# Optimization experiments

Hardware: AMD Instinct MI355X
Metric: run time of the kernel (lower is better)

## Reference

```python
import jax, jax.numpy as jnp
import numpy as np

HIDDEN = 1024
HEADS = 16
HEAD_DIM = HIDDEN // HEADS


def setup_inputs() -> dict:
    key = jax.random.key(0)
    k_x, k_wa, k_ba, k_wp, k_bp = jax.random.split(key, 5)
    x = jax.random.normal(k_x, (2, 2048, HIDDEN), dtype=jnp.float32)
    s_a = 1.0 / np.sqrt(HIDDEN)
    # torch Linear default init ~ U(-1/sqrt(fan_in), 1/sqrt(fan_in)); stored as [in, out]
    W_attn = jax.random.uniform(k_wa, (HIDDEN, 3 * HIDDEN), jnp.float32, -s_a, s_a)
    b_attn = jax.random.uniform(k_ba, (3 * HIDDEN,), jnp.float32, -s_a, s_a)
    W_proj = jax.random.uniform(k_wp, (HIDDEN, HIDDEN), jnp.float32, -s_a, s_a)
    b_proj = jax.random.uniform(k_bp, (HIDDEN,), jnp.float32, -s_a, s_a)
    return {"x": x, "W_attn": W_attn, "b_attn": b_attn, "W_proj": W_proj, "b_proj": b_proj}


def reference(x, W_attn, b_attn, W_proj, b_proj):
    B, S, D = x.shape
    H, Hd = HEADS, HEAD_DIM
    qkv = x @ W_attn + b_attn                     # [B, S, 3D]
    q, k, v = jnp.split(qkv, 3, axis=-1)
    # [B, H, S, Hd]
    q = q.reshape(B, S, H, Hd).transpose(0, 2, 1, 3)
    k = k.reshape(B, S, H, Hd).transpose(0, 2, 1, 3)
    v = v.reshape(B, S, H, Hd).transpose(0, 2, 1, 3)
    scale = 1.0 / np.sqrt(Hd).astype(np.float32)
    scores = jnp.einsum('bhqd,bhkd->bhqk', q, k) * scale   # [B, H, S, S]
    causal = jnp.triu(jnp.ones((S, S), dtype=bool), k=1)   # True above diagonal
    scores = jnp.where(causal, -jnp.inf, scores)
    probs = jax.nn.softmax(scores, axis=-1)
    # dropout p=0.0 -> identity (eval-mode equivalent)
    ctx = jnp.einsum('bhqk,bhkd->bhqd', probs, v)           # [B, H, S, Hd]
    ctx = ctx.transpose(0, 2, 1, 3).reshape(B, S, D)
    return ctx @ W_proj + b_proj
```

## Files before the change

kernel.cpp:

```cpp
#include <hip/hip_runtime.h>
#include <hip/hip_bf16.h>
#include <stdint.h>

#define HID 1024
#define NH 16
#define HD 64
#define SEQ 2048
#define BATCH 2
#define M_TOT 4096
#define QSCALE 0.18033688011112042f

typedef __attribute__((ext_vector_type(8))) short short8;
typedef __attribute__((ext_vector_type(4))) float f32x4;
typedef __attribute__((ext_vector_type(16))) float f32x16;
typedef __hip_bfloat16 bf16;

__device__ __forceinline__ void load_lds16(const void* g, void* l) {
  __builtin_amdgcn_global_load_lds(
      (const __attribute__((address_space(1))) unsigned int*)g,
      (__attribute__((address_space(3))) unsigned int*)l, 16, 0, 0);
}

__device__ __forceinline__ unsigned short f2bf_bits(float f) {
  __hip_bfloat16 h = __float2bfloat16(f);
  return *reinterpret_cast<unsigned short*>(&h);
}
__device__ __forceinline__ unsigned pack2bf(float a, float b) {
  return (unsigned)f2bf_bits(a) | ((unsigned)f2bf_bits(b) << 16);
}
__device__ __forceinline__ unsigned cvt_pk_bf16(float a, float b) {
  unsigned r;
  asm("v_cvt_pk_bf16_f32 %0, %1, %2" : "=v"(r) : "v"(a), "v"(b));
  return r;
}

__global__ void cvt_f32_to_bf16(const float* __restrict__ in,
                                bf16* __restrict__ out, int n4) {
  int i = blockIdx.x * blockDim.x + threadIdx.x;
  if (i >= n4) return;
  float4 v = reinterpret_cast<const float4*>(in)[i];
  ushort4 o;
  o.x = f2bf_bits(v.x); o.y = f2bf_bits(v.y);
  o.z = f2bf_bits(v.z); o.w = f2bf_bits(v.w);
  reinterpret_cast<ushort4*>(out)[i] = o;
}

__global__ void transpose_cvt2(const float* __restrict__ Wa, bf16* __restrict__ WTa,
                               const float* __restrict__ Wp, bf16* __restrict__ WTp) {
  __shared__ float tile[32][33];
  int bx = blockIdx.x;
  const float* W; bf16* WT; int N;
  if (bx < 96) { W = Wa; WT = WTa; N = 3072; }
  else         { W = Wp; WT = WTp; N = 1024; bx -= 96; }
  const int K = 1024;
  int n0 = bx * 32, k0 = blockIdx.y * 32;
  int tx = threadIdx.x, ty = threadIdx.y;
#pragma unroll
  for (int i = 0; i < 32; i += 8)
    tile[ty + i][tx] = W[(size_t)(k0 + ty + i) * N + n0 + tx];
  __syncthreads();
#pragma unroll
  for (int i = 0; i < 32; i += 8)
    WT[(size_t)(n0 + ty + i) * K + k0 + tx] = __float2bfloat16(tile[tx][ty + i]);
}

template <int EPI>
__global__ __launch_bounds__(256, 2)
void gemm128(const bf16* __restrict__ A, const bf16* __restrict__ BT,
             const float* __restrict__ bias,
             bf16* __restrict__ Qo, bf16* __restrict__ Ko, bf16* __restrict__ Vo,
             float* __restrict__ Fo) {
  const int Kdim = 1024;
  __shared__ bf16 As[128 * 64];
  __shared__ bf16 Bs[128 * 64];
  const int tid = threadIdx.x;
  const int wid = tid >> 6, lane = tid & 63;
  const int m0 = blockIdx.x * 128;
  const int n0 = blockIdx.y * 128;
  const int wrow = (wid >> 1) * 64, wcol = (wid & 1) * 64;

  f32x4 acc[4][4];
#pragma unroll
  for (int rb = 0; rb < 4; ++rb)
#pragma unroll
    for (int cb = 0; cb < 4; ++cb)
      acc[rb][cb] = (f32x4){0.f, 0.f, 0.f, 0.f};

  const int lr = lane >> 3;
  const int cc = lane & 7;
  const int lc = cc * 8;
  const int fr = lane & 15, fk = (lane >> 4) * 8;

  for (int kt = 0; kt < Kdim / 64; ++kt) {
    __syncthreads();
#pragma unroll
    for (int t = 0; t < 4; ++t) {
      int i = wid * 4 + t;
      int row = i * 8 + lr;
      load_lds16(A + (size_t)(m0 + row) * Kdim + kt * 64 + lc, (char*)As + i * 1024);
      load_lds16(BT + (size_t)(n0 + row) * Kdim + kt * 64 + lc, (char*)Bs + i * 1024);
    }
    __syncthreads();

    short8 af[4][2], bf_[4][2];
#pragma unroll
    for (int rb = 0; rb < 4; ++rb)
#pragma unroll
      for (int kk = 0; kk < 2; ++kk) {
        af[rb][kk] = *(const short8*)&As[(wrow + rb * 16 + fr) * 64 + kk * 32 + fk];
        bf_[rb][kk] = *(const short8*)&Bs[(wcol + rb * 16 + fr) * 64 + kk * 32 + fk];
      }
#pragma unroll
    for (int rb = 0; rb < 4; ++rb)
#pragma unroll
      for (int cb = 0; cb < 4; ++cb)
#pragma unroll
        for (int kk = 0; kk < 2; ++kk)
          acc[rb][cb] = __builtin_amdgcn_mfma_f32_16x16x32_bf16(
              af[rb][kk], bf_[cb][kk], acc[rb][cb], 0, 0, 0);
  }

  const int fg = (lane >> 4) * 4;
  float bv[4];
#pragma unroll
  for (int cb = 0; cb < 4; ++cb) bv[cb] = bias[n0 + wcol + cb * 16 + fr];

  if (EPI == 0) {
    __syncthreads();
    char* ep = (wid < 2 ? (char*)As : (char*)Bs) + (wid & 1) * 8192;
    const int ncol = n0 + wcol;
    const int part = ncol >> 10;
    const int h = (ncol & 1023) >> 6;
    const int b = m0 >> 11;
    const int s_base = (m0 + wrow) & 2047;
    const size_t hb = (size_t)(b * NH + h);

    if (part < 2) {
      const float qs = (part == 0) ? QSCALE : 1.f;
#pragma unroll
      for (int rb = 0; rb < 4; ++rb)
#pragma unroll
        for (int cb = 0; cb < 4; ++cb)
#pragma unroll
          for (int j = 0; j < 4; ++j) {
            int row = rb * 16 + fg + j;
            int colb = (cb * 16 + fr) * 2;
            *(unsigned short*)(ep + row * 128 + (colb ^ ((row & 7) << 4))) =
                f2bf_bits((acc[rb][cb][j] + bv[cb]) * qs);
          }
      bf16* dst = (part == 0 ? Qo : Ko) + hb * SEQ * HD;
#pragma unroll
      for (int p = 0; p < 8; ++p) {
        int row = p * 8 + lr;
        uint4 v = *(const uint4*)(ep + row * 128 + ((cc * 16) ^ ((row & 7) << 4)));
        *(uint4*)(dst + (size_t)(s_base + row) * HD + cc * 8) = v;
      }
    } else {
#pragma unroll
      for (int rb = 0; rb < 4; ++rb)
#pragma unroll
        for (int cb = 0; cb < 4; ++cb) {
          int cV = cb * 16 + fr;
          int r0 = (rb * 16 + fg) * 2;
          uint2 wv;
          wv.x = pack2bf(acc[rb][cb][0] + bv[cb], acc[rb][cb][1] + bv[cb]);
          wv.y = pack2bf(acc[rb][cb][2] + bv[cb], acc[rb][cb][3] + bv[cb]);
          *(uint2*)(ep + cV * 128 + (r0 ^ ((cV & 7) << 4))) = wv;
        }
      bf16* dstV = Vo + hb * HD * SEQ;
#pragma unroll
      for (int p = 0; p < 8; ++p) {
        int hd = p * 8 + lr;
        uint4 v = *(const uint4*)(ep + hd * 128 + ((cc * 16) ^ ((hd & 7) << 4)));
        *(uint4*)(dstV + (size_t)hd * SEQ + s_base + cc * 8) = v;
      }
    }
  } else {
#pragma unroll
    for (int rb = 0; rb < 4; ++rb) {
      int r0 = m0 + wrow + rb * 16 + fg;
#pragma unroll
      for (int cb = 0; cb < 4; ++cb) {
        int n = n0 + wcol + cb * 16 + fr;
#pragma unroll
        for (int j = 0; j < 4; ++j)
          Fo[(size_t)(r0 + j) * HID + n] = acc[rb][cb][j] + bv[cb];
      }
    }
  }
}

__global__ __launch_bounds__(256, 2)
void attn_kernel(const bf16* __restrict__ Q, const bf16* __restrict__ K,
                 const bf16* __restrict__ VT, bf16* __restrict__ ctx) {
  __shared__ char smem[65536];
  const int tid = threadIdx.x, wid = tid >> 6, lane = tid & 63;
  const int idx = blockIdx.x;
  const int qt = (idx < 256) ? (15 - (idx >> 5)) : ((idx - 256) >> 5);
  const int bh = idx & 31;
  const int b = bh >> 4, h = bh & 15;
  const size_t base = (size_t)bh * SEQ * HD;
  const int q0 = qt * 128 + wid * 32;

  const int fr = lane & 31, hi = lane >> 5;
  const int lr = lane >> 3;
  const int cc = lane & 7;
  const int qg = q0 + fr;
  const int gc = (cc ^ lr) * 8;

  short8 qf[4];
  const bf16* qp = Q + base + (size_t)qg * HD;
#pragma unroll
  for (int kc = 0; kc < 4; ++kc)
    qf[kc] = *(const short8*)(qp + kc * 16 + hi * 8);

  f32x16 oa[2], ob[2];
#pragma unroll
  for (int da = 0; da < 2; ++da)
#pragma unroll
    for (int r = 0; r < 16; ++r) { oa[da][r] = 0.f; ob[da][r] = 0.f; }
  float lpart = 0.f;

  auto stage_pair = [&](int jp) {
    char* nb = smem + (jp & 1) * 32768;
    const int nv = jp * 128;
#pragma unroll
    for (int u = 0; u < 2; ++u)
#pragma unroll
      for (int t = 0; t < 2; ++t) {
        int i = wid * 2 + t;
        load_lds16(K + base + (size_t)(nv + u * 64 + i * 8 + lr) * HD + gc,
                   nb + u * 16384 + i * 1024);
        load_lds16(VT + base + (size_t)(i * 8 + lr) * SEQ + nv + u * 64 + gc,
                   nb + u * 16384 + 8192 + i * 1024);
      }
  };

  auto tile_compute = [&](const char* sb_t, int kv0, f32x16 (&oc)[2]) {
    f32x16 sa[2];
    __builtin_amdgcn_s_setprio(1);
#pragma unroll
    for (int kb = 0; kb < 2; ++kb) {
#pragma unroll
      for (int r = 0; r < 16; ++r) sa[kb][r] = 0.f;
      const int row = kb * 32 + fr;
      const int swz = (row & 7) << 4;
#pragma unroll
      for (int kc = 0; kc < 4; ++kc) {
        short8 kf = *(const short8*)(sb_t + row * 128 + ((kc * 32 + hi * 16) ^ swz));
        sa[kb] = __builtin_amdgcn_mfma_f32_32x32x16_bf16(kf, qf[kc], sa[kb], 0, 0, 0);
      }
    }
    __builtin_amdgcn_s_setprio(0);

    if (kv0 + 63 > q0) {
#pragma unroll
      for (int kb = 0; kb < 2; ++kb)
#pragma unroll
        for (int r = 0; r < 16; ++r) {
          int kvg = kv0 + kb * 32 + (r & 3) + 8 * (r >> 2) + 4 * hi;
          sa[kb][r] = (kvg > qg) ? -1e30f : sa[kb][r];
        }
    }

    float s0 = 0.f, s1 = 0.f, s2 = 0.f, s3 = 0.f;
#pragma unroll
    for (int kb = 0; kb < 2; ++kb)
#pragma unroll
      for (int r = 0; r < 16; ++r) {
        float e = __builtin_exp2f(sa[kb][r]);
        sa[kb][r] = e;
        if ((r & 3) == 0)      s0 += e;
        else if ((r & 3) == 1) s1 += e;
        else if ((r & 3) == 2) s2 += e;
        else                   s3 += e;
      }
    lpart += (s0 + s1) + (s2 + s3);

    unsigned pk[2][8];
#pragma unroll
    for (int kb = 0; kb < 2; ++kb)
#pragma unroll
      for (int i = 0; i < 8; ++i)
        pk[kb][i] = cvt_pk_bf16(sa[kb][2 * i], sa[kb][2 * i + 1]);

    short8 pfr[4];
#pragma unroll
    for (int ks = 0; ks < 4; ++ks) {
      const int kb = ks >> 1, g = (ks & 1) * 4;
      auto r0 = __builtin_amdgcn_permlane32_swap((int)pk[kb][g + 0],
                                                 (int)pk[kb][g + 2], false, false);
      auto r1 = __builtin_amdgcn_permlane32_swap((int)pk[kb][g + 1],
                                                 (int)pk[kb][g + 3], false, false);
      union { unsigned u[4]; short8 s; } pf;
      pf.u[0] = (unsigned)r0[0]; pf.u[1] = (unsigned)r1[0];
      pf.u[2] = (unsigned)r0[1]; pf.u[3] = (unsigned)r1[1];
      pfr[ks] = pf.s;
    }

    __builtin_amdgcn_s_setprio(1);
#pragma unroll
    for (int da = 0; da < 2; ++da) {
      const int row = da * 32 + fr;
      const int swz = (row & 7) << 4;
#pragma unroll
      for (int ks = 0; ks < 4; ++ks) {
        short8 vf = *(const short8*)(sb_t + 8192 + row * 128 +
                                     ((ks * 32 + hi * 16) ^ swz));
        oc[da] = __builtin_amdgcn_mfma_f32_32x32x16_bf16(vf, pfr[ks], oc[da], 0, 0, 0);
      }
    }
    __builtin_amdgcn_s_setprio(0);
  };

  const int npair = qt + 1;

  stage_pair(0);

  for (int j = 0; j < npair; ++j) {
    char* sb = smem + (j & 1) * 32768;

    __builtin_amdgcn_s_barrier();
    __builtin_amdgcn_sched_barrier(0);

    if (j + 1 < npair) {
      stage_pair(j + 1);
      asm volatile("s_waitcnt vmcnt(8)" ::: "memory");
    } else {
      asm volatile("s_waitcnt vmcnt(0)" ::: "memory");
    }
    __builtin_amdgcn_sched_barrier(0);

    __builtin_amdgcn_s_barrier();
    __builtin_amdgcn_sched_barrier(0);

    const int kv0 = j * 128;
    if (kv0 <= q0 + 31)      tile_compute(sb,         kv0,      oa);
    if (kv0 + 64 <= q0 + 31) tile_compute(sb + 16384, kv0 + 64, ob);
  }

  const float lrun = lpart + __shfl_xor(lpart, 32);
  const float inv = 1.f / lrun;
  char* ep = smem + wid * 4096;
#pragma unroll
  for (int da = 0; da < 2; ++da)
#pragma unroll
    for (int rg = 0; rg < 4; ++rg) {
      int d0 = da * 64 + rg * 16 + hi * 8;
      float v0 = (oa[da][rg * 4 + 0] + ob[da][rg * 4 + 0]) * inv;
      float v1 = (oa[da][rg * 4 + 1] + ob[da][rg * 4 + 1]) * inv;
      float v2 = (oa[da][rg * 4 + 2] + ob[da][rg * 4 + 2]) * inv;
      float v3 = (oa[da][rg * 4 + 3] + ob[da][rg * 4 + 3]) * inv;
      uint2 wv; wv.x = pack2bf(v0, v1); wv.y = pack2bf(v2, v3);
      *(uint2*)(ep + fr * 128 + (d0 ^ ((fr & 7) << 4))) = wv;
    }
#pragma unroll
  for (int p = 0; p < 4; ++p) {
    int qr = p * 8 + lr;
    uint4 v = *(const uint4*)(ep + qr * 128 + ((cc * 16) ^ ((qr & 7) << 4)));
    int s = q0 + qr;
    *(uint4*)(ctx + (size_t)(b * SEQ + s) * HID + h * 64 + cc * 8) = v;
  }
}

extern "C" void kernel_launch(void* const* d_in, const int* in_sizes, int n_in,
                              void* d_out, int out_size, void* d_ws, size_t ws_size,
                              hipStream_t stream) {
  const float* x      = (const float*)d_in[0];
  const float* W_attn = (const float*)d_in[1];
  const float* b_attn = (const float*)d_in[2];
  const float* W_proj = (const float*)d_in[3];
  const float* b_proj = (const float*)d_in[4];
  float* out = (float*)d_out;

  char* ws = (char*)d_ws;
  const size_t MB = 1u << 20;
  bf16* xb   = (bf16*)(ws + 0);
  bf16* WTa  = (bf16*)(ws + 8 * MB);
  bf16* WTp  = (bf16*)(ws + 14 * MB);
  bf16* Qw   = (bf16*)(ws + 16 * MB);
  bf16* Kw   = (bf16*)(ws + 24 * MB);
  bf16* VTw  = (bf16*)(ws + 32 * MB);
  bf16* ctxb = (bf16*)(ws + 40 * MB);

  cvt_f32_to_bf16<<<(M_TOT * HID / 4 + 255) / 256, 256, 0, stream>>>(x, xb, M_TOT * HID / 4);
  transpose_cvt2<<<dim3(128, 32), dim3(32, 8), 0, stream>>>(W_attn, WTa, W_proj, WTp);

  gemm128<0><<<dim3(M_TOT / 128, 3 * HID / 128), 256, 0, stream>>>(
      xb, WTa, b_attn, Qw, Kw, VTw, nullptr);

  attn_kernel<<<dim3(512), 256, 0, stream>>>(Qw, Kw, VTw, ctxb);

  gemm128<1><<<dim3(M_TOT / 128, HID / 128), 256, 0, stream>>>(
      ctxb, WTp, b_proj, nullptr, nullptr, nullptr, out);
}
```

Measured before the change: 109.3 us.

## Shrink attention tiles to 64 queries with 16x16x32 MFMA and LDS-staged P

Restructures the attention kernel so each block handles 64 query rows instead of 128, with each wave owning 16 rows and using 16x16x32 bf16 MFMAs instead of 32x32x16. The grid doubles to 1024 blocks, LDS drops to 40 KB and launch bounds allow 4 blocks per CU, aiming for better occupancy and finer causal load balance. The probability fragment is now passed through LDS rather than permlane swaps, and K/V staging goes one 64-key tile at a time. The cost is more K/V reloads per query, since each KV tile is now reused across fewer queries, plus extra LDS traffic for P.

```diff
diff --git a/kernel.cpp b/kernel.cpp
--- a/kernel.cpp
+++ b/kernel.cpp
@@ -12,7 +12,6 @@
 
 typedef __attribute__((ext_vector_type(8))) short short8;
 typedef __attribute__((ext_vector_type(4))) float f32x4;
-typedef __attribute__((ext_vector_type(16))) float f32x16;
 typedef __hip_bfloat16 bf16;
 
 __device__ __forceinline__ void load_lds16(const void* g, void* l) {
@@ -190,142 +189,131 @@
   }
 }
 
-__global__ __launch_bounds__(256, 2)
+__global__ __launch_bounds__(256, 4)
 void attn_kernel(const bf16* __restrict__ Q, const bf16* __restrict__ K,
                  const bf16* __restrict__ VT, bf16* __restrict__ ctx) {
-  __shared__ char smem[65536];
+  __shared__ char smem[40960];
   const int tid = threadIdx.x, wid = tid >> 6, lane = tid & 63;
   const int idx = blockIdx.x;
-  const int qt = (idx < 256) ? (15 - (idx >> 5)) : ((idx - 256) >> 5);
+  const int qt = (idx < 512) ? (31 - (idx >> 5)) : ((idx - 512) >> 5);
   const int bh = idx & 31;
   const int b = bh >> 4, h = bh & 15;
   const size_t base = (size_t)bh * SEQ * HD;
-  const int q0 = qt * 128 + wid * 32;
-
-  const int fr = lane & 31, hi = lane >> 5;
+  const int q0 = qt * 64 + wid * 16;
+
+  const int fr16 = lane & 15, hi4 = lane >> 4;
   const int lr = lane >> 3;
   const int cc = lane & 7;
-  const int qg = q0 + fr;
+  const int qg = q0 + fr16;
   const int gc = (cc ^ lr) * 8;
-
-  short8 qf[4];
+  const int pswz = (fr16 & 7) << 4;
+  char* pp = smem + 32768 + wid * 2048;
+
+  short8 qf[2];
   const bf16* qp = Q + base + (size_t)qg * HD;
 #pragma unroll
-  for (int kc = 0; kc < 4; ++kc)
-    qf[kc] = *(const short8*)(qp + kc * 16 + hi * 8);
-
-  f32x16 oa[2], ob[2];
-#pragma unroll
-  for (int da = 0; da < 2; ++da)
-#pragma unroll
-    for (int r = 0; r < 16; ++r) { oa[da][r] = 0.f; ob[da][r] = 0.f; }
+  for (int kc = 0; kc < 2; ++kc)
+    qf[kc] = *(const short8*)(qp + kc * 32 + hi4 * 8);
+
+  f32x4 oa[4], ob[4];
+#pragma unroll
+  for (int dg = 0; dg < 4; ++dg) {
+    oa[dg] = (f32x4){0.f, 0.f, 0.f, 0.f};
+    ob[dg] = (f32x4){0.f, 0.f, 0.f, 0.f};
+  }
   float lpart = 0.f;
 
-  auto stage_pair = [&](int jp) {
-    char* nb = smem + (jp & 1) * 32768;
-    const int nv = jp * 128;
-#pragma unroll
-    for (int u = 0; u < 2; ++u)
-#pragma unroll
-      for (int t = 0; t < 2; ++t) {
-        int i = wid * 2 + t;
-        load_lds16(K + base + (size_t)(nv + u * 64 + i * 8 + lr) * HD + gc,
-                   nb + u * 16384 + i * 1024);
-        load_lds16(VT + base + (size_t)(i * 8 + lr) * SEQ + nv + u * 64 + gc,
-                   nb + u * 16384 + 8192 + i * 1024);
-      }
+  auto stage_tile = [&](int tt) {
+    char* nb = smem + (tt & 1) * 16384;
+    const int nv = tt * 64;
+#pragma unroll
+    for (int t = 0; t < 4; ++t) {
+      int c = wid * 4 + t;
+      if (c < 8)
+        load_lds16(K + base + (size_t)(nv + c * 8 + lr) * HD + gc, nb + c * 1024);
+      else
+        load_lds16(VT + base + (size_t)((c - 8) * 8 + lr) * SEQ + nv + gc,
+                   nb + 8192 + (c - 8) * 1024);
+    }
   };
 
-  auto tile_compute = [&](const char* sb_t, int kv0, f32x16 (&oc)[2]) {
-    f32x16 sa[2];
+  auto tile_compute = [&](const char* sb, int kv0, f32x4 (&oc)[4]) {
+    f32x4 sa[4];
     __builtin_amdgcn_s_setprio(1);
 #pragma unroll
-    for (int kb = 0; kb < 2; ++kb) {
-#pragma unroll
-      for (int r = 0; r < 16; ++r) sa[kb][r] = 0.f;
-      const int row = kb * 32 + fr;
+    for (int kb = 0; kb < 4; ++kb) {
+      sa[kb] = (f32x4){0.f, 0.f, 0.f, 0.f};
+      const int row = kb * 16 + fr16;
       const int swz = (row & 7) << 4;
 #pragma unroll
-      for (int kc = 0; kc < 4; ++kc) {
-        short8 kf = *(const short8*)(sb_t + row * 128 + ((kc * 32 + hi * 16) ^ swz));
-        sa[kb] = __builtin_amdgcn_mfma_f32_32x32x16_bf16(kf, qf[kc], sa[kb], 0, 0, 0);
+      for (int kc = 0; kc < 2; ++kc) {
+        short8 kf = *(const short8*)(sb + row * 128 + ((kc * 64 + hi4 * 16) ^ swz));
+        sa[kb] = __builtin_amdgcn_mfma_f32_16x16x32_bf16(kf, qf[kc], sa[kb], 0, 0, 0);
       }
     }
     __builtin_amdgcn_s_setprio(0);
 
     if (kv0 + 63 > q0) {
 #pragma unroll
-      for (int kb = 0; kb < 2; ++kb)
-#pragma unroll
-        for (int r = 0; r < 16; ++r) {
-          int kvg = kv0 + kb * 32 + (r & 3) + 8 * (r >> 2) + 4 * hi;
-          sa[kb][r] = (kvg > qg) ? -1e30f : sa[kb][r];
+      for (int kb = 0; kb < 4; ++kb)
+#pragma unroll
+        for (int j = 0; j < 4; ++j) {
+          int kvg = kv0 + kb * 16 + hi4 * 4 + j;
+          sa[kb][j] = (kvg > qg) ? -1e30f : sa[kb][j];
         }
     }
 
     float s0 = 0.f, s1 = 0.f, s2 = 0.f, s3 = 0.f;
 #pragma unroll
-    for (int kb = 0; kb < 2; ++kb)
-#pragma unroll
-      for (int r = 0; r < 16; ++r) {
-        float e = __builtin_exp2f(sa[kb][r]);
-        sa[kb][r] = e;
-        if ((r & 3) == 0)      s0 += e;
-        else if ((r & 3) == 1) s1 += e;
-        else if ((r & 3) == 2) s2 += e;
-        else                   s3 += e;
-      }
+    for (int kb = 0; kb < 4; ++kb) {
+      float e0 = __builtin_exp2f(sa[kb][0]);
+      float e1 = __builtin_exp2f(sa[kb][1]);
+      float e2 = __builtin_exp2f(sa[kb][2]);
+      float e3 = __builtin_exp2f(sa[kb][3]);
+      sa[kb][0] = e0; sa[kb][1] = e1; sa[kb][2] = e2; sa[kb][3] = e3;
+      s0 += e0; s1 += e1; s2 += e2; s3 += e3;
+    }
     lpart += (s0 + s1) + (s2 + s3);
 
-    unsigned pk[2][8];
-#pragma unroll
-    for (int kb = 0; kb < 2; ++kb)
-#pragma unroll
-      for (int i = 0; i < 8; ++i)
-        pk[kb][i] = cvt_pk_bf16(sa[kb][2 * i], sa[kb][2 * i + 1]);
-
-    short8 pfr[4];
-#pragma unroll
-    for (int ks = 0; ks < 4; ++ks) {
-      const int kb = ks >> 1, g = (ks & 1) * 4;
-      auto r0 = __builtin_amdgcn_permlane32_swap((int)pk[kb][g + 0],
-                                                 (int)pk[kb][g + 2], false, false);
-      auto r1 = __builtin_amdgcn_permlane32_swap((int)pk[kb][g + 1],
-                                                 (int)pk[kb][g + 3], false, false);
-      union { unsigned u[4]; short8 s; } pf;
-      pf.u[0] = (unsigned)r0[0]; pf.u[1] = (unsigned)r1[0];
-      pf.u[2] = (unsigned)r0[1]; pf.u[3] = (unsigned)r1[1];
-      pfr[ks] = pf.s;
-    }
-
+#pragma unroll
+    for (int kb = 0; kb < 4; ++kb) {
+      uint2 u;
+      u.x = cvt_pk_bf16(sa[kb][0], sa[kb][1]);
+      u.y = cvt_pk_bf16(sa[kb][2], sa[kb][3]);
+      *(uint2*)(pp + fr16 * 128 + ((kb * 32 + hi4 * 8) ^ pswz)) = u;
+    }
+    short8 pfrag[2];
+#pragma unroll
+    for (int ks = 0; ks < 2; ++ks)
+      pfrag[ks] = *(const short8*)(pp + fr16 * 128 + ((ks * 64 + hi4 * 16) ^ pswz));
+
+    const char* sv = sb + 8192;
     __builtin_amdgcn_s_setprio(1);
 #pragma unroll
-    for (int da = 0; da < 2; ++da) {
-      const int row = da * 32 + fr;
-      const int swz = (row & 7) << 4;
-#pragma unroll
-      for (int ks = 0; ks < 4; ++ks) {
-        short8 vf = *(const short8*)(sb_t + 8192 + row * 128 +
-                                     ((ks * 32 + hi * 16) ^ swz));
-        oc[da] = __builtin_amdgcn_mfma_f32_32x32x16_bf16(vf, pfr[ks], oc[da], 0, 0, 0);
+    for (int dg = 0; dg < 4; ++dg) {
+      const int row = dg * 16 + fr16;
+#pragma unroll
+      for (int ks = 0; ks < 2; ++ks) {
+        short8 vf = *(const short8*)(sv + row * 128 + ((ks * 64 + hi4 * 16) ^ pswz));
+        oc[dg] = __builtin_amdgcn_mfma_f32_16x16x32_bf16(vf, pfrag[ks], oc[dg], 0, 0, 0);
       }
     }
     __builtin_amdgcn_s_setprio(0);
   };
 
-  const int npair = qt + 1;
-
-  stage_pair(0);
-
-  for (int j = 0; j < npair; ++j) {
-    char* sb = smem + (j & 1) * 32768;
+  const int ntiles = qt + 1;
+
+  stage_tile(0);
+
+  for (int t = 0; t < ntiles; ++t) {
+    const char* sb = smem + (t & 1) * 16384;
 
     __builtin_amdgcn_s_barrier();
     __builtin_amdgcn_sched_barrier(0);
 
-    if (j + 1 < npair) {
-      stage_pair(j + 1);
-      asm volatile("s_waitcnt vmcnt(8)" ::: "memory");
+    if (t + 1 < ntiles) {
+      stage_tile(t + 1);
+      asm volatile("s_waitcnt vmcnt(4)" ::: "memory");
     } else {
       asm volatile("s_waitcnt vmcnt(0)" ::: "memory");
     }
@@ -334,30 +322,29 @@
     __builtin_amdgcn_s_barrier();
     __builtin_amdgcn_sched_barrier(0);
 
-    const int kv0 = j * 128;
-    if (kv0 <= q0 + 31)      tile_compute(sb,         kv0,      oa);
-    if (kv0 + 64 <= q0 + 31) tile_compute(sb + 16384, kv0 + 64, ob);
-  }
-
-  const float lrun = lpart + __shfl_xor(lpart, 32);
+    const int kv0 = t * 64;
+    if (kv0 <= q0 + 15) {
+      if (t & 1) tile_compute(sb, kv0, ob);
+      else       tile_compute(sb, kv0, oa);
+    }
+  }
+
+  float lrun = lpart + __shfl_xor(lpart, 16);
+  lrun += __shfl_xor(lrun, 32);
   const float inv = 1.f / lrun;
-  char* ep = smem + wid * 4096;
-#pragma unroll
-  for (int da = 0; da < 2; ++da)
-#pragma unroll
-    for (int rg = 0; rg < 4; ++rg) {
-      int d0 = da * 64 + rg * 16 + hi * 8;
-      float v0 = (oa[da][rg * 4 + 0] + ob[da][rg * 4 + 0]) * inv;
-      float v1 = (oa[da][rg * 4 + 1] + ob[da][rg * 4 + 1]) * inv;
-      float v2 = (oa[da][rg * 4 + 2] + ob[da][rg * 4 + 2]) * inv;
-      float v3 = (oa[da][rg * 4 + 3] + ob[da][rg * 4 + 3]) * inv;
-      uint2 wv; wv.x = pack2bf(v0, v1); wv.y = pack2bf(v2, v3);
-      *(uint2*)(ep + fr * 128 + (d0 ^ ((fr & 7) << 4))) = wv;
-    }
-#pragma unroll
-  for (int p = 0; p < 4; ++p) {
+#pragma unroll
+  for (int dg = 0; dg < 4; ++dg) {
+    float v0 = (oa[dg][0] + ob[dg][0]) * inv;
+    float v1 = (oa[dg][1] + ob[dg][1]) * inv;
+    float v2 = (oa[dg][2] + ob[dg][2]) * inv;
+    float v3 = (oa[dg][3] + ob[dg][3]) * inv;
+    uint2 wv; wv.x = pack2bf(v0, v1); wv.y = pack2bf(v2, v3);
+    *(uint2*)(pp + fr16 * 128 + ((dg * 32 + hi4 * 8) ^ pswz)) = wv;
+  }
+#pragma unroll
+  for (int p = 0; p < 2; ++p) {
     int qr = p * 8 + lr;
-    uint4 v = *(const uint4*)(ep + qr * 128 + ((cc * 16) ^ ((qr & 7) << 4)));
+    uint4 v = *(const uint4*)(pp + qr * 128 + ((cc * 16) ^ ((qr & 7) << 4)));
     int s = q0 + qr;
     *(uint4*)(ctx + (size_t)(b * SEQ + s) * HID + h * 64 + cc * 8) = v;
   }
@@ -389,7 +376,7 @@
   gemm128<0><<<dim3(M_TOT / 128, 3 * HID / 128), 256, 0, stream>>>(
       xb, WTa, b_attn, Qw, Kw, VTw, nullptr);
 
-  attn_kernel<<<dim3(512), 256, 0, stream>>>(Qw, Kw, VTw, ctxb);
+  attn_kernel<<<dim3(1024), 256, 0, stream>>>(Qw, Kw, VTw, ctxb);
 
   gemm128<1><<<dim3(M_TOT / 128, HID / 128), 256, 0, stream>>>(
       ctxb, WTp, b_proj, nullptr, nullptr, nullptr, out);
```

Measured after the change: 115.5 us. 1.06x slower.

## Double-buffer GEMM LDS tiles to overlap global loads with MFMA

Applied to the files above, without the earlier changes.

The gemm128 kernel now keeps two LDS tile buffers (64 KB total). It issues the global-to-LDS loads for the next k-tile before computing on the current one, using explicit vmcnt waits and barriers instead of a load-then-compute sequence. It also raises wave priority around the MFMA block. The aim is to hide global memory latency behind matrix math. The cost is doubled LDS, which may limit the launch_bounds(256,2) occupancy, and correctness now rests on hand-counted vmcnt values.

```diff
diff --git a/kernel.cpp b/kernel.cpp
--- a/kernel.cpp
+++ b/kernel.cpp
@@ -71,8 +71,7 @@
              bf16* __restrict__ Qo, bf16* __restrict__ Ko, bf16* __restrict__ Vo,
              float* __restrict__ Fo) {
   const int Kdim = 1024;
-  __shared__ bf16 As[128 * 64];
-  __shared__ bf16 Bs[128 * 64];
+  __shared__ char smem[65536];
   const int tid = threadIdx.x;
   const int wid = tid >> 6, lane = tid & 63;
   const int m0 = blockIdx.x * 128;
@@ -91,16 +90,37 @@
   const int lc = cc * 8;
   const int fr = lane & 15, fk = (lane >> 4) * 8;
 
-  for (int kt = 0; kt < Kdim / 64; ++kt) {
-    __syncthreads();
+  auto stage = [&](int kt) {
+    char* nb = smem + (kt & 1) * 32768;
 #pragma unroll
     for (int t = 0; t < 4; ++t) {
       int i = wid * 4 + t;
       int row = i * 8 + lr;
-      load_lds16(A + (size_t)(m0 + row) * Kdim + kt * 64 + lc, (char*)As + i * 1024);
-      load_lds16(BT + (size_t)(n0 + row) * Kdim + kt * 64 + lc, (char*)Bs + i * 1024);
-    }
-    __syncthreads();
+      load_lds16(A + (size_t)(m0 + row) * Kdim + kt * 64 + lc, nb + i * 1024);
+      load_lds16(BT + (size_t)(n0 + row) * Kdim + kt * 64 + lc,
+                 nb + 16384 + i * 1024);
+    }
+  };
+
+  stage(0);
+
+  for (int kt = 0; kt < Kdim / 64; ++kt) {
+    const bf16* As = (const bf16*)(smem + (kt & 1) * 32768);
+    const bf16* Bs = As + 8192;
+
+    __builtin_amdgcn_s_barrier();
+    __builtin_amdgcn_sched_barrier(0);
+
+    if (kt + 1 < Kdim / 64) {
+      stage(kt + 1);
+      asm volatile("s_waitcnt vmcnt(8)" ::: "memory");
+    } else {
+      asm volatile("s_waitcnt vmcnt(0)" ::: "memory");
+    }
+    __builtin_amdgcn_sched_barrier(0);
+
+    __builtin_amdgcn_s_barrier();
+    __builtin_amdgcn_sched_barrier(0);
 
     short8 af[4][2], bf_[4][2];
 #pragma unroll
@@ -110,6 +130,7 @@
         af[rb][kk] = *(const short8*)&As[(wrow + rb * 16 + fr) * 64 + kk * 32 + fk];
         bf_[rb][kk] = *(const short8*)&Bs[(wcol + rb * 16 + fr) * 64 + kk * 32 + fk];
       }
+    __builtin_amdgcn_s_setprio(1);
 #pragma unroll
     for (int rb = 0; rb < 4; ++rb)
 #pragma unroll
@@ -118,6 +139,7 @@
         for (int kk = 0; kk < 2; ++kk)
           acc[rb][cb] = __builtin_amdgcn_mfma_f32_16x16x32_bf16(
               af[rb][kk], bf_[cb][kk], acc[rb][cb], 0, 0, 0);
+    __builtin_amdgcn_s_setprio(0);
   }
 
   const int fg = (lane >> 4) * 4;
@@ -127,7 +149,7 @@
 
   if (EPI == 0) {
     __syncthreads();
-    char* ep = (wid < 2 ? (char*)As : (char*)Bs) + (wid & 1) * 8192;
+    char* ep = smem + wid * 8192;
     const int ncol = n0 + wcol;
     const int part = ncol >> 10;
     const int h = (ncol & 1023) >> 6;
```

New measurement: 108.6 us. No clear change (-0.6%).
